# Optimization experiments

Measured on AMD Instinct MI355X. Metric: run time of the kernel, lower is better.

Reference implementation:

```python
import jax, jax.numpy as jnp
import numpy as np
import math

B, Q, D = 2, 2048, 1024
H, R = 16, 12
DH = D // H
RHO = 2.0
MAX_OFFSET = 6.0


def setup_inputs() -> dict:
    key = jax.random.key(0)
    ks = jax.random.split(key, 16)
    s = 0.02
    inp = {
        'x': jax.random.normal(ks[0], (B, Q, D), dtype=jnp.float32),
        'wq': jax.random.normal(ks[1], (D, D), dtype=jnp.float32) * s,
        'bq': jnp.zeros((D,), jnp.float32),
        'wk': jax.random.normal(ks[2], (D, D), dtype=jnp.float32) * s,
        'bk': jnp.zeros((D,), jnp.float32),
        'wv': jax.random.normal(ks[3], (D, D), dtype=jnp.float32) * s,
        'bv': jnp.zeros((D,), jnp.float32),
        'wo': jax.random.normal(ks[4], (D, D), dtype=jnp.float32) * s,
        'bo': jnp.zeros((D,), jnp.float32),
        'dw_w': jax.random.normal(ks[5], (D, 1, 3), dtype=jnp.float32) * s,  # depthwise conv1d k=3
        'dw_b': jnp.zeros((D,), jnp.float32),
        'pw_w': jax.random.normal(ks[6], (H * R, D), dtype=jnp.float32) * s,  # pointwise conv1d k=1
        'pw_b': jnp.zeros((H * R,), jnp.float32),
        'rel_scale': jnp.asarray(0.1, jnp.float32),
    }
    return inp


def _split_heads(y):
    b, q, d = y.shape
    return y.reshape(b, q, H, DH).transpose(0, 2, 1, 3)  # (b,h,q,dh)


def _sample(seq, pos):
    # seq: (b,h,q,dh), pos: (b,h,q,r) fractional positions -> (b,h,q,r,dh)
    b, h, q, dh = seq.shape
    low = jnp.clip(jnp.floor(pos), 0, q - 1).astype(jnp.int32)
    high = jnp.clip(jnp.ceil(pos), 0, q - 1).astype(jnp.int32)
    frac = (pos - low.astype(pos.dtype))[..., None]
    bi = jnp.arange(b)[:, None, None, None]
    hi = jnp.arange(h)[None, :, None, None]
    gl = seq[bi, hi, low]   # (b,h,q,r,dh) gather
    gh = seq[bi, hi, high]
    return gl * (1.0 - frac) + gh * frac


def reference(x, wq, bq, wk, bk, wv, bv, wo, bo, dw_w, dw_b, pw_w, pw_b, rel_scale):
    b, q, d = x.shape
    q_lin = x @ wq.T + bq
    qh = _split_heads(q_lin)
    kh = _split_heads(x @ wk.T + bk)
    vh = _split_heads(x @ wv.T + bv)

    # learned offsets: depthwise conv (k=3, groups=d) -> gelu -> pointwise conv
    feat = q_lin.transpose(0, 2, 1)  # (b,d,q)
    dw = jax.lax.conv_general_dilated(
        feat, dw_w, window_strides=(1,), padding=[(1, 1)],
        feature_group_count=D, dimension_numbers=('NCH', 'OIH', 'NCH'))
    dw = dw + dw_b[None, :, None]
    g = jax.nn.gelu(dw, approximate=False)
    off = jnp.einsum('od,bdq->boq', pw_w, g) + pw_b[None, :, None]  # (b,h*r,q)
    off = off.transpose(0, 2, 1).reshape(b, q, H, R).transpose(0, 2, 1, 3)  # (b,h,q,r)
    off = jnp.tanh(off) * MAX_OFFSET

    base = jnp.arange(q, dtype=x.dtype)[None, None, :, None]
    anchor = jnp.linspace(-RHO, RHO, R, dtype=x.dtype)[None, None, None, :]
    positions = jnp.clip(base + anchor + off, 0.0, q - 1.0)  # (b,h,q,r)

    sk = _sample(kh, positions)  # (b,h,q,r,dh)
    sv = _sample(vh, positions)

    scores = jnp.einsum('bhqd,bhqrd->bhqr', qh, sk) / math.sqrt(DH)
    rel = positions - jnp.arange(q, dtype=x.dtype)[None, None, :, None]
    scores = scores - rel_scale * jnp.abs(rel)
    attn = jax.nn.softmax(scores, axis=-1)
    out = jnp.einsum('bhqr,bhqrd->bhqd', attn, sv)  # (b,h,q,dh)
    out = out.transpose(0, 2, 1, 3).reshape(b, q, d)
    return out @ wo.T + bo
```

## Files before the change

### kernel.cpp

```cpp
#include <hip/hip_runtime.h>
#include <math.h>

constexpr int B_  = 2;
constexpr int Q_  = 2048;
constexpr int D_  = 1024;
constexpr int H_  = 16;
constexpr int R_  = 12;
constexpr int DH_ = 64;
constexpr int M_  = B_ * Q_;
constexpr int HR_ = H_ * R_;
constexpr int NQKV = 3 * D_;

typedef short bf16x8 __attribute__((ext_vector_type(8)));
typedef float f32x4  __attribute__((ext_vector_type(4)));

__device__ __forceinline__ float bf2f(unsigned short u) {
    return __uint_as_float(((unsigned)u) << 16);
}
__device__ __forceinline__ unsigned short f2bf(float f) {
    unsigned u = __float_as_uint(f);
    return (unsigned short)((u + 0x7fffu + ((u >> 16) & 1u)) >> 16);
}

__global__ __launch_bounds__(256) void cvt_all(const float* __restrict__ x,
                                               const float* __restrict__ wq,
                                               const float* __restrict__ wk,
                                               const float* __restrict__ wv,
                                               const float* __restrict__ wo,
                                               const float* __restrict__ pww,
                                               const float* __restrict__ bq,
                                               const float* __restrict__ bk,
                                               const float* __restrict__ bv,
                                               unsigned short* __restrict__ xb,
                                               unsigned short* __restrict__ wqkv,
                                               unsigned short* __restrict__ wob,
                                               unsigned short* __restrict__ pwwb,
                                               float* __restrict__ bqkv) {
    const int blk = blockIdx.x;
    if (blk >= 4192) {
        const int i = (blk - 4192) * 256 + threadIdx.x;
        bqkv[i] = i < D_ ? bq[i] : (i < 2 * D_ ? bk[i - D_] : bv[i - 2 * D_]);
        return;
    }
    const int i = blk * 256 + threadIdx.x;
    const float* src;
    unsigned short* dst;
    int rel;
    if (i < 524288)       { src = x;   dst = xb;                          rel = i; }
    else if (i < 655360)  { src = wq;  dst = wqkv;                        rel = i - 524288; }
    else if (i < 786432)  { src = wk;  dst = wqkv + (size_t)D_ * D_;      rel = i - 655360; }
    else if (i < 917504)  { src = wv;  dst = wqkv + (size_t)2 * D_ * D_;  rel = i - 786432; }
    else if (i < 1048576) { src = wo;  dst = wob;                         rel = i - 917504; }
    else                  { src = pww; dst = pwwb;                        rel = i - 1048576; }

    const float4 a = ((const float4*)src)[2 * rel];
    const float4 b = ((const float4*)src)[2 * rel + 1];
    uint4 o;
    o.x = (unsigned)f2bf(a.x) | ((unsigned)f2bf(a.y) << 16);
    o.y = (unsigned)f2bf(a.z) | ((unsigned)f2bf(a.w) << 16);
    o.z = (unsigned)f2bf(b.x) | ((unsigned)f2bf(b.y) << 16);
    o.w = (unsigned)f2bf(b.z) | ((unsigned)f2bf(b.w) << 16);
    ((uint4*)dst)[rel] = o;
}

template <int BN, bool OUT_BF16>
__global__ __launch_bounds__(256) void gemm_mfma(const unsigned short* __restrict__ A,
                                                 const unsigned short* __restrict__ W,
                                                 const float* __restrict__ bias,
                                                 void* __restrict__ Cv,
                                                 int M, int N, int K) {
    constexpr int BM  = 128, BK = 64;
    constexpr int FN  = BN / 32;
    constexpr int CHA = BM / 8;
    constexpr int CHB = BN / 8;
    __shared__ unsigned short As[BM * BK];
    __shared__ unsigned short Bs[BN * BK];

    const int tid  = threadIdx.x;
    const int w    = tid >> 6, lane = tid & 63;
    const int wm   = w >> 1,   wn   = w & 1;

    const int nbx = gridDim.x;
    const int cpx = nbx >> 3;
    const int orig = blockIdx.y * nbx + blockIdx.x;
    const int xcd  = orig & 7;
    const int idx  = orig >> 3;
    const int bm = (idx / cpx) * BM;
    const int bn = (xcd * cpx + idx % cpx) * BN;

    const int srow  = lane >> 3;
    const int sslot = (lane & 7) ^ (srow & 7);
    const int fr = lane & 15;
    const int s  = lane >> 4;
    const int fx = fr & 7;

    f32x4 acc[4][FN];
    #pragma unroll
    for (int i = 0; i < 4; ++i)
        #pragma unroll
        for (int j = 0; j < FN; ++j) acc[i][j] = (f32x4){0.f, 0.f, 0.f, 0.f};

    for (int k0 = 0; k0 < K; k0 += BK) {
        __syncthreads();
        #pragma unroll
        for (int c = w; c < CHA; c += 4) {
            const unsigned short* g = A + (size_t)(bm + c * 8 + srow) * K + k0 + sslot * 8;
            __builtin_amdgcn_global_load_lds(
                (const __attribute__((address_space(1))) void*)g,
                (__attribute__((address_space(3))) void*)((char*)As + c * 1024), 16, 0, 0);
        }
        #pragma unroll
        for (int c = w; c < CHB; c += 4) {
            const unsigned short* g = W + (size_t)(bn + c * 8 + srow) * K + k0 + sslot * 8;
            __builtin_amdgcn_global_load_lds(
                (const __attribute__((address_space(1))) void*)g,
                (__attribute__((address_space(3))) void*)((char*)Bs + c * 1024), 16, 0, 0);
        }
        __syncthreads();

        #pragma unroll
        for (int ks = 0; ks < 2; ++ks) {
            const int sl = (((ks << 2) | s) ^ fx) * 8;
            bf16x8 af[4];
            #pragma unroll
            for (int i = 0; i < 4; ++i)
                af[i] = *(const bf16x8*)(As + (wm * 64 + i * 16 + fr) * BK + sl);
            #pragma unroll
            for (int j = 0; j < FN; ++j) {
                const bf16x8 bfrag = *(const bf16x8*)(Bs + (wn * (BN / 2) + j * 16 + fr) * BK + sl);
                #pragma unroll
                for (int i = 0; i < 4; ++i)
                    acc[i][j] = __builtin_amdgcn_mfma_f32_16x16x32_bf16(af[i], bfrag, acc[i][j], 0, 0, 0);
            }
        }
    }

    #pragma unroll
    for (int j = 0; j < FN; ++j) {
        const int col = bn + wn * (BN / 2) + j * 16 + fr;
        const float bv = bias[col];
        #pragma unroll
        for (int i = 0; i < 4; ++i) {
            const int row0 = bm + wm * 64 + i * 16 + ((lane >> 4) << 2);
            #pragma unroll
            for (int ii = 0; ii < 4; ++ii) {
                const float v = acc[i][j][ii] + bv;
                if constexpr (OUT_BF16)
                    ((unsigned short*)Cv)[(size_t)(row0 + ii) * N + col] = f2bf(v);
                else
                    ((float*)Cv)[(size_t)(row0 + ii) * N + col] = v;
            }
        }
    }
}

__global__ __launch_bounds__(256) void dwpw_kernel(const unsigned short* __restrict__ qkv,
                                                   const float* __restrict__ dww,
                                                   const float* __restrict__ dwb,
                                                   const unsigned short* __restrict__ pwwb,
                                                   const float* __restrict__ pwb,
                                                   unsigned short* __restrict__ offb) {
    __shared__ unsigned short As[16 * 1024];
    __shared__ unsigned short Bs[192 * 64];
    const int tid  = threadIdx.x;
    const int w    = tid >> 6, lane = tid & 63;
    const int m0   = blockIdx.x * 16;

    for (int u = tid; u < 16 * 128; u += 256) {
        const int r  = u >> 7;
        const int c8 = (u & 127) << 3;
        const int m  = m0 + r;
        const int t  = m & (Q_ - 1);
        const unsigned short* row = qkv + (size_t)m * NQKV + c8;

        unsigned short cur[8], prv[8] = {0}, nxt[8] = {0};
        *(uint4*)cur = *(const uint4*)row;
        if (t > 0)      *(uint4*)prv = *(const uint4*)(row - NQKV);
        if (t < Q_ - 1) *(uint4*)nxt = *(const uint4*)(row + NQKV);

        float dwl[24];
        #pragma unroll
        for (int q2 = 0; q2 < 6; ++q2)
            *(f32x4*)&dwl[q2 * 4] = *(const f32x4*)&dww[c8 * 3 + q2 * 4];
        float db[8];
        *(f32x4*)&db[0] = *(const f32x4*)&dwb[c8];
        *(f32x4*)&db[4] = *(const f32x4*)&dwb[c8 + 4];

        unsigned short o[8];
        #pragma unroll
        for (int j = 0; j < 8; ++j) {
            float v = bf2f(prv[j]) * dwl[j * 3 + 0] + bf2f(cur[j]) * dwl[j * 3 + 1]
                    + bf2f(nxt[j]) * dwl[j * 3 + 2] + db[j];
            v = 0.5f * v * (1.0f + erff(v * 0.70710678118654752f));
            o[j] = f2bf(v);
        }
        const int slot = (c8 >> 3) ^ (r & 7);
        *(uint4*)(As + r * 1024 + slot * 8) = *(uint4*)o;
    }
    __syncthreads();

    const int srow  = lane >> 3;
    const int sslot = (lane & 7) ^ (srow & 7);
    const int fr = lane & 15;
    const int s  = lane >> 4;
    const int fx = fr & 7;

    f32x4 acc[3];
    #pragma unroll
    for (int j = 0; j < 3; ++j) acc[j] = (f32x4){0.f, 0.f, 0.f, 0.f};

    for (int k0 = 0; k0 < 1024; k0 += 64) {
        if (k0) __syncthreads();
        #pragma unroll
        for (int c = w; c < 24; c += 4) {
            const unsigned short* g = pwwb + (size_t)(c * 8 + srow) * 1024 + k0 + sslot * 8;
            __builtin_amdgcn_global_load_lds(
                (const __attribute__((address_space(1))) void*)g,
                (__attribute__((address_space(3))) void*)((char*)Bs + c * 1024), 16, 0, 0);
        }
        __syncthreads();

        #pragma unroll
        for (int ks = 0; ks < 2; ++ks) {
            const int aslot = ((k0 >> 3) + ((ks << 2) | s)) ^ fx;
            const bf16x8 af = *(const bf16x8*)(As + fr * 1024 + aslot * 8);
            const int sl = (((ks << 2) | s) ^ fx) * 8;
            #pragma unroll
            for (int j = 0; j < 3; ++j) {
                const bf16x8 bfrag = *(const bf16x8*)(Bs + (w * 48 + j * 16 + fr) * 64 + sl);
                acc[j] = __builtin_amdgcn_mfma_f32_16x16x32_bf16(af, bfrag, acc[j], 0, 0, 0);
            }
        }
    }

    #pragma unroll
    for (int j = 0; j < 3; ++j) {
        const int n = w * 48 + j * 16 + fr;
        const float bv = pwb[n];
        const int row0 = (lane >> 4) << 2;
        #pragma unroll
        for (int ii = 0; ii < 4; ++ii)
            offb[(size_t)(m0 + row0 + ii) * HR_ + n] = f2bf(acc[j][ii] + bv);
    }
}

__global__ __launch_bounds__(256) void coeff_pv_kernel(const unsigned short* __restrict__ qkv,
                                                       const unsigned short* __restrict__ offb,
                                                       const float* __restrict__ rel_scale_p,
                                                       unsigned short* __restrict__ attb) {
    __shared__ __align__(16) float S[4][16][33];
    __shared__ __align__(16) float C[4][16][32];
    const int tid  = threadIdx.x;
    const int w    = tid >> 6, lane = tid & 63;
    const int tile = blockIdx.x * 4 + w;
    const int t0   = (tile & 127) << 4;
    const int h    = (tile >> 7) & 15;
    const int b    = tile >> 11;
    const int fr   = lane & 15;
    const int fo   = (lane >> 4) << 3;

    const unsigned short* qrow = qkv + (size_t)(b * Q_ + t0 + fr) * NQKV + h * DH_ + fo;
    const bf16x8 af0 = *(const bf16x8*)qrow;
    const bf16x8 af1 = *(const bf16x8*)(qrow + 32);

    f32x4 acc0 = (f32x4){0.f, 0.f, 0.f, 0.f};
    f32x4 acc1 = acc0;
    {
        int j = min(max(t0 - 8 + fr, 0), Q_ - 1);
        const unsigned short* krow = qkv + (size_t)(b * Q_ + j) * NQKV + D_ + h * DH_ + fo;
        acc0 = __builtin_amdgcn_mfma_f32_16x16x32_bf16(af0, *(const bf16x8*)krow, acc0, 0, 0, 0);
        acc0 = __builtin_amdgcn_mfma_f32_16x16x32_bf16(af1, *(const bf16x8*)(krow + 32), acc0, 0, 0, 0);
    }
    {
        int j = min(max(t0 + 8 + fr, 0), Q_ - 1);
        const unsigned short* krow = qkv + (size_t)(b * Q_ + j) * NQKV + D_ + h * DH_ + fo;
        acc1 = __builtin_amdgcn_mfma_f32_16x16x32_bf16(af0, *(const bf16x8*)krow, acc1, 0, 0, 0);
        acc1 = __builtin_amdgcn_mfma_f32_16x16x32_bf16(af1, *(const bf16x8*)(krow + 32), acc1, 0, 0, 0);
    }

    float vj[32];
    {
        const unsigned short* vb = qkv + (size_t)b * Q_ * NQKV + 2 * D_ + h * DH_ + lane;
        #pragma unroll
        for (int i2 = 0; i2 < 32; ++i2) {
            const int j = min(max(t0 - 8 + i2, 0), Q_ - 1);
            vj[i2] = bf2f(vb[(size_t)j * NQKV]);
        }
    }

    const int row0 = (lane >> 4) << 2;
    #pragma unroll
    for (int ii = 0; ii < 4; ++ii) {
        S[w][row0 + ii][fr]      = acc0[ii];
        S[w][row0 + ii][16 + fr] = acc1[ii];
    }
    {
        const int tr = lane >> 2, cg = (lane & 3) << 3;
        #pragma unroll
        for (int k = 0; k < 8; ++k) C[w][tr][cg + k] = 0.f;
    }
    __syncthreads();

    const int tloc = lane & 15;
    const int rs   = lane >> 4;
    const int t    = t0 + tloc;
    const float rel_scale = rel_scale_p[0];
    const unsigned short* offrow = offb + (size_t)(b * Q_ + t) * HR_ + h * R_;

    float sc[3], fr3[3];
    int   cl[3], ch[3];
    #pragma unroll
    for (int i = 0; i < 3; ++i) {
        const int r = rs * 3 + i;
        const float off    = bf2f(offrow[r]);
        const float anchor = -2.0f + (4.0f / 11.0f) * (float)r;
        float pos = (float)t + anchor + 6.0f * tanhf(off);
        pos = fminf(fmaxf(pos, 0.0f), (float)(Q_ - 1));
        const float fl = floorf(pos);
        const int lo = (int)fl;
        const int hi = (int)ceilf(pos);
        const float f = pos - fl;
        cl[i] = lo - t0 + 8;
        ch[i] = hi - t0 + 8;
        fr3[i] = f;
        const float slo = S[w][tloc][cl[i]];
        const float shi = S[w][tloc][ch[i]];
        sc[i] = (slo * (1.0f - f) + shi * f) * 0.125f - rel_scale * fabsf(pos - (float)t);
    }

    float mx = fmaxf(fmaxf(sc[0], sc[1]), sc[2]);
    mx = fmaxf(mx, __shfl_xor(mx, 16));
    mx = fmaxf(mx, __shfl_xor(mx, 32));
    float e[3];
    #pragma unroll
    for (int i = 0; i < 3; ++i) e[i] = expf(sc[i] - mx);
    float sum = e[0] + e[1] + e[2];
    sum += __shfl_xor(sum, 16);
    sum += __shfl_xor(sum, 32);
    const float inv = 1.0f / sum;

    #pragma unroll
    for (int i = 0; i < 3; ++i) {
        const float wgt = e[i] * inv;
        atomicAdd(&C[w][tloc][cl[i]], wgt * (1.0f - fr3[i]));
        atomicAdd(&C[w][tloc][ch[i]], wgt * fr3[i]);
    }
    __syncthreads();

    #pragma unroll
    for (int tl = 0; tl < 16; ++tl) {
        const int st = tl & ~3;
        float cw[20];
        #pragma unroll
        for (int q2 = 0; q2 < 5; ++q2)
            *(f32x4*)&cw[q2 * 4] = *(const f32x4*)&C[w][tl][st + q2 * 4];
        float acc2 = 0.f;
        #pragma unroll
        for (int k = 0; k <= 16; ++k)
            acc2 = fmaf(cw[tl - st + k], vj[tl + k], acc2);
        attb[(size_t)(b * Q_ + t0 + tl) * D_ + h * DH_ + lane] = f2bf(acc2);
    }
}

extern "C" void kernel_launch(void* const* d_in, const int* in_sizes, int n_in,
                              void* d_out, int out_size, void* d_ws, size_t ws_size,
                              hipStream_t stream) {
    const float* x    = (const float*)d_in[0];
    const float* wq   = (const float*)d_in[1];
    const float* bq   = (const float*)d_in[2];
    const float* wk   = (const float*)d_in[3];
    const float* bk   = (const float*)d_in[4];
    const float* wv   = (const float*)d_in[5];
    const float* bv   = (const float*)d_in[6];
    const float* wo   = (const float*)d_in[7];
    const float* bo   = (const float*)d_in[8];
    const float* dww  = (const float*)d_in[9];
    const float* dwb  = (const float*)d_in[10];
    const float* pww  = (const float*)d_in[11];
    const float* pwb  = (const float*)d_in[12];
    const float* rsc  = (const float*)d_in[13];
    float* out = (float*)d_out;

    unsigned short* xb   = (unsigned short*)d_ws;
    unsigned short* wqkv = xb   + (size_t)M_ * D_;
    unsigned short* wob  = wqkv + (size_t)NQKV * D_;
    unsigned short* pwwb = wob  + (size_t)D_ * D_;
    unsigned short* qkv  = pwwb + (size_t)HR_ * D_;
    unsigned short* offb = qkv  + (size_t)M_ * NQKV;
    unsigned short* attb = offb + (size_t)M_ * HR_;
    float*          bqkv = (float*)(attb + (size_t)M_ * D_);

    dim3 blk(256);

    hipLaunchKernelGGL(cvt_all, dim3(4204), blk, 0, stream,
                       x, wq, wk, wv, wo, pww, bq, bk, bv, xb, wqkv, wob, pwwb, bqkv);

    hipLaunchKernelGGL((gemm_mfma<128, true>), dim3(NQKV / 128, M_ / 128), blk, 0, stream,
                       xb, wqkv, bqkv, qkv, M_, NQKV, D_);

    hipLaunchKernelGGL(dwpw_kernel, dim3(M_ / 16), blk, 0, stream,
                       qkv, dww, dwb, pwwb, pwb, offb);

    hipLaunchKernelGGL(coeff_pv_kernel, dim3(B_ * H_ * (Q_ / 16) / 4), blk, 0, stream,
                       qkv, offb, rsc, attb);

    hipLaunchKernelGGL((gemm_mfma<64, false>), dim3(D_ / 64, M_ / 128), blk, 0, stream,
                       attb, wob, bo, out, M_, D_, D_);
}
```

Measured before the change: 97.86 us.

## Double-buffer LDS tiles in GEMM and pointwise-conv kernels to overlap loads

Shared-memory A/B tiles in the bf16 MFMA GEMM, and the weight tiles in the depthwise+pointwise kernel, become two-stage ping-pong buffers. The next K tile is issued via global_load_lds before computing on the current one, which removes one barrier per iteration and hides global load latency behind MFMA work. The dwpw kernel also prefetches its first weight tile before the depthwise/GELU phase. The cost is doubled LDS use, which may reduce occupancy, and reliance on the barrier waiting for the async LDS loads to finish.

```diff
diff --git a/kernel.cpp b/kernel.cpp
--- a/kernel.cpp
+++ b/kernel.cpp
@@ -73,8 +73,8 @@
     constexpr int FN  = BN / 32;
     constexpr int CHA = BM / 8;
     constexpr int CHB = BN / 8;
-    __shared__ unsigned short As[BM * BK];
-    __shared__ unsigned short Bs[BN * BK];
+    __shared__ unsigned short As[2][BM * BK];
+    __shared__ unsigned short Bs[2][BN * BK];
 
     const int tid  = threadIdx.x;
     const int w    = tid >> 6, lane = tid & 63;
@@ -94,46 +94,54 @@
     const int s  = lane >> 4;
     const int fx = fr & 7;
 
+#define STAGE_TILE(buf, k0)                                                     \
+    {                                                                           \
+        _Pragma("unroll")                                                       \
+        for (int c = w; c < CHA; c += 4) {                                      \
+            const unsigned short* g = A + (size_t)(bm + c * 8 + srow) * K + (k0) + sslot * 8; \
+            __builtin_amdgcn_global_load_lds(                                   \
+                (const __attribute__((address_space(1))) void*)g,               \
+                (__attribute__((address_space(3))) void*)((char*)As[buf] + c * 1024), 16, 0, 0); \
+        }                                                                       \
+        _Pragma("unroll")                                                       \
+        for (int c = w; c < CHB; c += 4) {                                      \
+            const unsigned short* g = W + (size_t)(bn + c * 8 + srow) * K + (k0) + sslot * 8; \
+            __builtin_amdgcn_global_load_lds(                                   \
+                (const __attribute__((address_space(1))) void*)g,               \
+                (__attribute__((address_space(3))) void*)((char*)Bs[buf] + c * 1024), 16, 0, 0); \
+        }                                                                       \
+    }
+
     f32x4 acc[4][FN];
     #pragma unroll
     for (int i = 0; i < 4; ++i)
         #pragma unroll
         for (int j = 0; j < FN; ++j) acc[i][j] = (f32x4){0.f, 0.f, 0.f, 0.f};
 
+    STAGE_TILE(0, 0)
+    __syncthreads();
+    int cur = 0;
     for (int k0 = 0; k0 < K; k0 += BK) {
-        __syncthreads();
-        #pragma unroll
-        for (int c = w; c < CHA; c += 4) {
-            const unsigned short* g = A + (size_t)(bm + c * 8 + srow) * K + k0 + sslot * 8;
-            __builtin_amdgcn_global_load_lds(
-                (const __attribute__((address_space(1))) void*)g,
-                (__attribute__((address_space(3))) void*)((char*)As + c * 1024), 16, 0, 0);
-        }
-        #pragma unroll
-        for (int c = w; c < CHB; c += 4) {
-            const unsigned short* g = W + (size_t)(bn + c * 8 + srow) * K + k0 + sslot * 8;
-            __builtin_amdgcn_global_load_lds(
-                (const __attribute__((address_space(1))) void*)g,
-                (__attribute__((address_space(3))) void*)((char*)Bs + c * 1024), 16, 0, 0);
-        }
-        __syncthreads();
-
+        if (k0 + BK < K) STAGE_TILE(cur ^ 1, k0 + BK)
         #pragma unroll
         for (int ks = 0; ks < 2; ++ks) {
             const int sl = (((ks << 2) | s) ^ fx) * 8;
             bf16x8 af[4];
             #pragma unroll
             for (int i = 0; i < 4; ++i)
-                af[i] = *(const bf16x8*)(As + (wm * 64 + i * 16 + fr) * BK + sl);
+                af[i] = *(const bf16x8*)(As[cur] + (wm * 64 + i * 16 + fr) * BK + sl);
             #pragma unroll
             for (int j = 0; j < FN; ++j) {
-                const bf16x8 bfrag = *(const bf16x8*)(Bs + (wn * (BN / 2) + j * 16 + fr) * BK + sl);
+                const bf16x8 bfrag = *(const bf16x8*)(Bs[cur] + (wn * (BN / 2) + j * 16 + fr) * BK + sl);
                 #pragma unroll
                 for (int i = 0; i < 4; ++i)
                     acc[i][j] = __builtin_amdgcn_mfma_f32_16x16x32_bf16(af[i], bfrag, acc[i][j], 0, 0, 0);
             }
         }
-    }
+        __syncthreads();
+        cur ^= 1;
+    }
+#undef STAGE_TILE
 
     #pragma unroll
     for (int j = 0; j < FN; ++j) {
@@ -161,10 +169,29 @@
                                                    const float* __restrict__ pwb,
                                                    unsigned short* __restrict__ offb) {
     __shared__ unsigned short As[16 * 1024];
-    __shared__ unsigned short Bs[192 * 64];
+    __shared__ unsigned short Bs[2][192 * 64];
     const int tid  = threadIdx.x;
     const int w    = tid >> 6, lane = tid & 63;
     const int m0   = blockIdx.x * 16;
+
+    const int srow  = lane >> 3;
+    const int sslot = (lane & 7) ^ (srow & 7);
+    const int fr = lane & 15;
+    const int s  = lane >> 4;
+    const int fx = fr & 7;
+
+#define STAGE_B(buf, k0)                                                        \
+    {                                                                           \
+        _Pragma("unroll")                                                       \
+        for (int c = w; c < 24; c += 4) {                                       \
+            const unsigned short* g = pwwb + (size_t)(c * 8 + srow) * 1024 + (k0) + sslot * 8; \
+            __builtin_amdgcn_global_load_lds(                                   \
+                (const __attribute__((address_space(1))) void*)g,               \
+                (__attribute__((address_space(3))) void*)((char*)Bs[buf] + c * 1024), 16, 0, 0); \
+        }                                                                       \
+    }
+
+    STAGE_B(0, 0)
 
     for (int u = tid; u < 16 * 128; u += 256) {
         const int r  = u >> 7;
@@ -199,27 +226,13 @@
     }
     __syncthreads();
 
-    const int srow  = lane >> 3;
-    const int sslot = (lane & 7) ^ (srow & 7);
-    const int fr = lane & 15;
-    const int s  = lane >> 4;
-    const int fx = fr & 7;
-
     f32x4 acc[3];
     #pragma unroll
     for (int j = 0; j < 3; ++j) acc[j] = (f32x4){0.f, 0.f, 0.f, 0.f};
 
+    int cur = 0;
     for (int k0 = 0; k0 < 1024; k0 += 64) {
-        if (k0) __syncthreads();
-        #pragma unroll
-        for (int c = w; c < 24; c += 4) {
-            const unsigned short* g = pwwb + (size_t)(c * 8 + srow) * 1024 + k0 + sslot * 8;
-            __builtin_amdgcn_global_load_lds(
-                (const __attribute__((address_space(1))) void*)g,
-                (__attribute__((address_space(3))) void*)((char*)Bs + c * 1024), 16, 0, 0);
-        }
-        __syncthreads();
-
+        if (k0 < 960) STAGE_B(cur ^ 1, k0 + 64)
         #pragma unroll
         for (int ks = 0; ks < 2; ++ks) {
             const int aslot = ((k0 >> 3) + ((ks << 2) | s)) ^ fx;
@@ -227,11 +240,14 @@
             const int sl = (((ks << 2) | s) ^ fx) * 8;
             #pragma unroll
             for (int j = 0; j < 3; ++j) {
-                const bf16x8 bfrag = *(const bf16x8*)(Bs + (w * 48 + j * 16 + fr) * 64 + sl);
+                const bf16x8 bfrag = *(const bf16x8*)(Bs[cur] + (w * 48 + j * 16 + fr) * 64 + sl);
                 acc[j] = __builtin_amdgcn_mfma_f32_16x16x32_bf16(af, bfrag, acc[j], 0, 0, 0);
             }
         }
-    }
+        __syncthreads();
+        cur ^= 1;
+    }
+#undef STAGE_B
 
     #pragma unroll
     for (int j = 0; j < 3; ++j) {
```

New measurement: 110.7 us. 1.13x slower.

## Stage GEMM epilogue through LDS and double-buffer pointwise weight loads

Applied to the files above, without the earlier changes.

The GEMM epilogue now adds bias, writes each wave's accumulator tile into padded shared memory, and reads it back as contiguous rows. Each lane then issues 16-byte global stores, replacing scattered scalar stores. The dwpw kernel gets a second shared buffer for the pointwise weights: the next K-slice is prefetched while the current one is used, and the first slice's load overlaps the depthwise/GELU stage. The cost is extra shared-memory traffic and footprint, plus one extra barrier in the GEMM.

```diff
diff --git a/kernel.cpp b/kernel.cpp
--- a/kernel.cpp
+++ b/kernel.cpp
@@ -73,8 +73,11 @@
     constexpr int FN  = BN / 32;
     constexpr int CHA = BM / 8;
     constexpr int CHB = BN / 8;
-    __shared__ unsigned short As[BM * BK];
-    __shared__ unsigned short Bs[BN * BK];
+    constexpr int WCOLS = BN / 2;
+    constexpr int CP = OUT_BF16 ? (WCOLS + 8) : (WCOLS + 4);
+    __shared__ unsigned short smem[(BM + BN) * BK];
+    unsigned short* As = smem;
+    unsigned short* Bs = smem + BM * BK;
 
     const int tid  = threadIdx.x;
     const int w    = tid >> 6, lane = tid & 63;
@@ -127,30 +130,67 @@
                 af[i] = *(const bf16x8*)(As + (wm * 64 + i * 16 + fr) * BK + sl);
             #pragma unroll
             for (int j = 0; j < FN; ++j) {
-                const bf16x8 bfrag = *(const bf16x8*)(Bs + (wn * (BN / 2) + j * 16 + fr) * BK + sl);
+                const bf16x8 bfrag = *(const bf16x8*)(Bs + (wn * WCOLS + j * 16 + fr) * BK + sl);
                 #pragma unroll
                 for (int i = 0; i < 4; ++i)
                     acc[i][j] = __builtin_amdgcn_mfma_f32_16x16x32_bf16(af[i], bfrag, acc[i][j], 0, 0, 0);
             }
         }
     }
-
-    #pragma unroll
-    for (int j = 0; j < FN; ++j) {
-        const int col = bn + wn * (BN / 2) + j * 16 + fr;
-        const float bv = bias[col];
-        #pragma unroll
-        for (int i = 0; i < 4; ++i) {
-            const int row0 = bm + wm * 64 + i * 16 + ((lane >> 4) << 2);
+    __syncthreads();
+
+    float biasv[FN];
+    #pragma unroll
+    for (int j = 0; j < FN; ++j) biasv[j] = bias[bn + wn * WCOLS + j * 16 + fr];
+
+    const int rl    = lane >> 1;
+    const int chalf = lane & 1;
+
+    #pragma unroll
+    for (int hf = 0; hf < 2; ++hf) {
+        #pragma unroll
+        for (int i2 = 0; i2 < 2; ++i2) {
+            const int i = hf * 2 + i2;
             #pragma unroll
-            for (int ii = 0; ii < 4; ++ii) {
-                const float v = acc[i][j][ii] + bv;
-                if constexpr (OUT_BF16)
-                    ((unsigned short*)Cv)[(size_t)(row0 + ii) * N + col] = f2bf(v);
-                else
-                    ((float*)Cv)[(size_t)(row0 + ii) * N + col] = v;
-            }
-        }
+            for (int j = 0; j < FN; ++j)
+                #pragma unroll
+                for (int ii = 0; ii < 4; ++ii) {
+                    const int rloc = i2 * 16 + s * 4 + ii;
+                    const int cloc = j * 16 + fr;
+                    const float v = acc[i][j][ii] + biasv[j];
+                    if constexpr (OUT_BF16)
+                        ((unsigned short*)smem)[w * 32 * CP + rloc * CP + cloc] = f2bf(v);
+                    else
+                        ((float*)smem)[w * 32 * CP + rloc * CP + cloc] = v;
+                }
+        }
+        asm volatile("s_waitcnt lgkmcnt(0)" ::: "memory");
+        if constexpr (OUT_BF16) {
+            const unsigned short* ep = (const unsigned short*)smem + w * 32 * CP + rl * CP + chalf * 32;
+            const uint4 q0 = *(const uint4*)(ep);
+            const uint4 q1 = *(const uint4*)(ep + 8);
+            const uint4 q2 = *(const uint4*)(ep + 16);
+            const uint4 q3 = *(const uint4*)(ep + 24);
+            unsigned short* dst = (unsigned short*)Cv
+                + (size_t)(bm + wm * 64 + hf * 32 + rl) * N + bn + wn * WCOLS + chalf * 32;
+            *(uint4*)(dst)      = q0;
+            *(uint4*)(dst + 8)  = q1;
+            *(uint4*)(dst + 16) = q2;
+            *(uint4*)(dst + 24) = q3;
+        } else {
+            const float* ep = (const float*)smem + w * 32 * CP + rl * CP + chalf * 16;
+            const float4 q0 = *(const float4*)(ep);
+            const float4 q1 = *(const float4*)(ep + 4);
+            const float4 q2 = *(const float4*)(ep + 8);
+            const float4 q3 = *(const float4*)(ep + 12);
+            float* dst = (float*)Cv
+                + (size_t)(bm + wm * 64 + hf * 32 + rl) * N + bn + wn * WCOLS + chalf * 16;
+            *(float4*)(dst)      = q0;
+            *(float4*)(dst + 4)  = q1;
+            *(float4*)(dst + 8)  = q2;
+            *(float4*)(dst + 12) = q3;
+        }
+        if (hf == 0) asm volatile("s_waitcnt lgkmcnt(0)" ::: "memory");
     }
 }
 
@@ -161,10 +201,29 @@
                                                    const float* __restrict__ pwb,
                                                    unsigned short* __restrict__ offb) {
     __shared__ unsigned short As[16 * 1024];
-    __shared__ unsigned short Bs[192 * 64];
+    __shared__ unsigned short Bs[2][192 * 64];
     const int tid  = threadIdx.x;
     const int w    = tid >> 6, lane = tid & 63;
     const int m0   = blockIdx.x * 16;
+
+    const int srow  = lane >> 3;
+    const int sslot = (lane & 7) ^ (srow & 7);
+    const int fr = lane & 15;
+    const int s  = lane >> 4;
+    const int fx = fr & 7;
+
+#define STAGE_B(buf, k0)                                                        \
+    {                                                                           \
+        _Pragma("unroll")                                                       \
+        for (int c = w; c < 24; c += 4) {                                       \
+            const unsigned short* g = pwwb + (size_t)(c * 8 + srow) * 1024 + (k0) + sslot * 8; \
+            __builtin_amdgcn_global_load_lds(                                   \
+                (const __attribute__((address_space(1))) void*)g,               \
+                (__attribute__((address_space(3))) void*)((char*)Bs[buf] + c * 1024), 16, 0, 0); \
+        }                                                                       \
+    }
+
+    STAGE_B(0, 0)
 
     for (int u = tid; u < 16 * 128; u += 256) {
         const int r  = u >> 7;
@@ -199,27 +258,13 @@
     }
     __syncthreads();
 
-    const int srow  = lane >> 3;
-    const int sslot = (lane & 7) ^ (srow & 7);
-    const int fr = lane & 15;
-    const int s  = lane >> 4;
-    const int fx = fr & 7;
-
     f32x4 acc[3];
     #pragma unroll
     for (int j = 0; j < 3; ++j) acc[j] = (f32x4){0.f, 0.f, 0.f, 0.f};
 
+    int cur = 0;
     for (int k0 = 0; k0 < 1024; k0 += 64) {
-        if (k0) __syncthreads();
-        #pragma unroll
-        for (int c = w; c < 24; c += 4) {
-            const unsigned short* g = pwwb + (size_t)(c * 8 + srow) * 1024 + k0 + sslot * 8;
-            __builtin_amdgcn_global_load_lds(
-                (const __attribute__((address_space(1))) void*)g,
-                (__attribute__((address_space(3))) void*)((char*)Bs + c * 1024), 16, 0, 0);
-        }
-        __syncthreads();
-
+        if (k0 < 960) STAGE_B(cur ^ 1, k0 + 64)
         #pragma unroll
         for (int ks = 0; ks < 2; ++ks) {
             const int aslot = ((k0 >> 3) + ((ks << 2) | s)) ^ fx;
@@ -227,11 +272,14 @@
             const int sl = (((ks << 2) | s) ^ fx) * 8;
             #pragma unroll
             for (int j = 0; j < 3; ++j) {
-                const bf16x8 bfrag = *(const bf16x8*)(Bs + (w * 48 + j * 16 + fr) * 64 + sl);
+                const bf16x8 bfrag = *(const bf16x8*)(Bs[cur] + (w * 48 + j * 16 + fr) * 64 + sl);
                 acc[j] = __builtin_amdgcn_mfma_f32_16x16x32_bf16(af, bfrag, acc[j], 0, 0, 0);
             }
         }
-    }
+        __syncthreads();
+        cur ^= 1;
+    }
+#undef STAGE_B
 
     #pragma unroll
     for (int j = 0; j < 3; ++j) {
```

Result: slower. 105.3 us (+7.6%).
